# Performance work log

Hardware: AMD Instinct MI355X
Metric: run time of the kernel (lower is better)

The kernel has to match this reference:

```python
import jax, jax.numpy as jnp
import numpy as np

B, H, W = 8, 64, 64
DIM, NH, WS = 384, 6, 14
HD = DIM // NH
MLP = int(DIM * 4.0)
EPS = 1e-5
SCALE = HD ** -0.5


def setup_inputs() -> dict:
    key = jax.random.key(0)
    ks = jax.random.split(key, 8)
    init = lambda k, shape: (jax.random.normal(k, shape, dtype=jnp.float32) * 0.02)
    return {
        "x": jax.random.normal(ks[0], (B, H, W, DIM), dtype=jnp.float32),
        "ln1_w": jnp.ones((DIM,), jnp.float32),
        "ln1_b": jnp.zeros((DIM,), jnp.float32),
        "qkv_w": init(ks[1], (DIM, 3 * DIM)),
        "qkv_b": jnp.zeros((3 * DIM,), jnp.float32),
        "proj_w": init(ks[2], (DIM, DIM)),
        "proj_b": jnp.zeros((DIM,), jnp.float32),
        "rel_pos_h": init(ks[3], (2 * WS - 1, HD)),
        "rel_pos_w": init(ks[4], (2 * WS - 1, HD)),
        "ln2_w": jnp.ones((DIM,), jnp.float32),
        "ln2_b": jnp.zeros((DIM,), jnp.float32),
        "fc1_w": init(ks[5], (DIM, MLP)),
        "fc1_b": jnp.zeros((MLP,), jnp.float32),
        "fc2_w": init(ks[6], (MLP, DIM)),
        "fc2_b": jnp.zeros((DIM,), jnp.float32),
    }


def _layernorm(x, w, b):
    m = x.mean(-1, keepdims=True)
    v = ((x - m) ** 2).mean(-1, keepdims=True)
    return (x - m) * jax.lax.rsqrt(v + EPS) * w + b


def _get_rel_pos(rel_pos, ws):
    # q_size == k_size == ws and rel_pos has 2*ws-1 rows, so torch's
    # F.interpolate to max_rel_dist=2*ws-1 is an identity; direct indexing.
    coords = jnp.arange(ws)[:, None] - jnp.arange(ws)[None, :] + (ws - 1)
    return rel_pos[coords]  # (ws, ws, head_dim)


def _attention(xw, qkv_w, qkv_b, proj_w, proj_b, rel_pos_h, rel_pos_w):
    Bw = xw.shape[0]
    N = WS * WS
    qkv = xw.reshape(Bw, N, DIM) @ qkv_w + qkv_b  # (Bw, N, 3*DIM)
    qkv = qkv.reshape(Bw, N, 3, NH, HD).transpose(2, 0, 3, 1, 4).reshape(3, Bw * NH, N, HD)
    q, k, v = qkv[0], qkv[1], qkv[2]
    attn = jnp.einsum("bqd,bkd->bqk", q * SCALE, k)  # (Bw*NH, N, N)
    Rh = _get_rel_pos(rel_pos_h, WS)
    Rw = _get_rel_pos(rel_pos_w, WS)
    rq = q.reshape(Bw * NH, WS, WS, HD)
    rel_h = jnp.einsum("bhwc,hkc->bhwk", rq, Rh)
    rel_w = jnp.einsum("bhwc,wkc->bhwk", rq, Rw)
    attn = (attn.reshape(Bw * NH, WS, WS, WS, WS)
            + rel_h[:, :, :, :, None]
            + rel_w[:, :, :, None, :]).reshape(Bw * NH, N, N)
    attn = jax.nn.softmax(attn, axis=-1)
    out = jnp.einsum("bqk,bkd->bqd", attn, v)
    out = out.reshape(Bw, NH, WS, WS, HD).transpose(0, 2, 3, 1, 4).reshape(Bw, WS, WS, DIM)
    return out @ proj_w + proj_b


def reference(x, ln1_w, ln1_b, qkv_w, qkv_b, proj_w, proj_b, rel_pos_h, rel_pos_w,
              ln2_w, ln2_b, fc1_w, fc1_b, fc2_w, fc2_b):
    shortcut = x
    h = _layernorm(x, ln1_w, ln1_b)
    pad_h = (WS - H % WS) % WS
    pad_w = (WS - W % WS) % WS
    Hp, Wp = H + pad_h, W + pad_w
    hp = jnp.pad(h, ((0, 0), (0, pad_h), (0, pad_w), (0, 0)))
    # window partition: (B, Hp, Wp, C) -> (B*nWin, WS, WS, C)
    wins = hp.reshape(B, Hp // WS, WS, Wp // WS, WS, DIM)
    wins = wins.transpose(0, 1, 3, 2, 4, 5).reshape(-1, WS, WS, DIM)
    wins = _attention(wins, qkv_w, qkv_b, proj_w, proj_b, rel_pos_h, rel_pos_w)
    # window unpartition
    y = wins.reshape(B, Hp // WS, Wp // WS, WS, WS, DIM)
    y = y.transpose(0, 1, 3, 2, 4, 5).reshape(B, Hp, Wp, DIM)[:, :H, :W, :]
    x = shortcut + y
    h2 = _layernorm(x, ln2_w, ln2_b)
    mlp = jax.nn.gelu(h2 @ fc1_w + fc1_b, approximate=False) @ fc2_w + fc2_b
    return x + mlp
```

## Files before the change

kernel.cpp:

```cpp
#include <hip/hip_runtime.h>
#include <math.h>

#define DIMC 384
#define NHD  6
#define HD   64
#define WSZ  14
#define NTOK 196
#define NWIN 200
#define NWH  1200
#define MWIN 39200
#define MX   32768
#define MLPD 1536

typedef short short8 __attribute__((ext_vector_type(8)));
typedef float f32x4 __attribute__((ext_vector_type(4)));
typedef float f32x16 __attribute__((ext_vector_type(16)));

__device__ __forceinline__ unsigned short f2bf(float f) {
  unsigned int u = __float_as_uint(f);
  u = (u + 0x7fffu + ((u >> 16) & 1u)) >> 16;
  return (unsigned short)u;
}
__device__ __forceinline__ unsigned int pkbf(float a, float b) {
  unsigned int r; asm("v_cvt_pk_bf16_f32 %0, %1, %2" : "=v"(r) : "v"(a), "v"(b)); return r;
}
__device__ __forceinline__ float gelu_t(float x) {
  float z = 1.5957691216057308f * (x + 0.044715f * x * x * x);
  float e = __expf(z);
  float th = 1.f - 2.f * __builtin_amdgcn_rcpf(e + 1.f);
  return 0.5f * x * (1.f + th);
}

typedef const __attribute__((address_space(1))) unsigned int* gptr_t;
typedef __attribute__((address_space(3))) unsigned int* lptr_t;
__device__ __forceinline__ void gload16(const unsigned short* g, unsigned short* l) {
  __builtin_amdgcn_global_load_lds((gptr_t)(const void*)g, (lptr_t)(void*)l, 16, 0, 0);
}

__global__ void wtrans_kernel(const float* __restrict__ in, unsigned short* __restrict__ out,
                              int K, int N) {
  int id = blockIdx.x * 256 + threadIdx.x;
  if (id >= K * N) return;
  int n = id / K, k = id - n * K;
  out[id] = f2bf(in[(size_t)k * N + n]);
}

__global__ void relprep_kernel(const float* __restrict__ relh, const float* __restrict__ relw,
                               unsigned short* __restrict__ relcat) {
  int id = blockIdx.x * 256 + threadIdx.x;
  if (id >= 64 * 64) return;
  int rc = id >> 6, d = id & 63;
  float v = 0.f;
  if (rc < 27) v = relh[rc * 64 + d] * 8.f;
  else if (rc < 54) v = relw[(rc - 27) * 64 + d] * 8.f;
  relcat[id] = f2bf(v);
}

__global__ void vpad_kernel(unsigned short* __restrict__ vT) {
  int id = blockIdx.x * 256 + threadIdx.x;
  if (id >= 76800 * 3) return;
  int row = id / 3, part = id - row * 3;
  *(int2*)(vT + (size_t)row * 208 + 196 + part * 4) = make_int2(0, 0);
}

__global__ __launch_bounds__(64) void ln1win_kernel(const float* __restrict__ x,
    const float* __restrict__ w, const float* __restrict__ b, unsigned short* __restrict__ xw) {
  int t = blockIdx.x;
  int lane = threadIdx.x;
  int win = t / NTOK, p = t - win * NTOK;
  int bb = win / 25, rem = win - bb * 25;
  int wi = rem / 5, wj = rem - wi * 5;
  int i = p / WSZ, j = p - i * WSZ;
  int r = wi * WSZ + i, c = wj * WSZ + j;
  unsigned short* o = xw + (size_t)t * DIMC;
  if (r >= 64 || c >= 64) {
    #pragma unroll
    for (int q = 0; q < 6; q++) o[lane + q * 64] = 0;
    return;
  }
  const float* xr = x + (((size_t)bb * 64 + r) * 64 + c) * DIMC;
  float v[6]; float s = 0.f, s2 = 0.f;
  #pragma unroll
  for (int q = 0; q < 6; q++) { float f = xr[lane + q * 64]; v[q] = f; s += f; s2 += f * f; }
  #pragma unroll
  for (int off = 32; off; off >>= 1) { s += __shfl_xor(s, off); s2 += __shfl_xor(s2, off); }
  float mean = s * (1.f / DIMC);
  float var  = s2 * (1.f / DIMC) - mean * mean;
  float rstd = rsqrtf(var + 1e-5f);
  #pragma unroll
  for (int q = 0; q < 6; q++) {
    int d = lane + q * 64;
    o[d] = f2bf((v[q] - mean) * rstd * w[d] + b[d]);
  }
}

__global__ __launch_bounds__(64) void ln2_kernel(const float* __restrict__ x2,
    const float* __restrict__ w, const float* __restrict__ b, unsigned short* __restrict__ h2) {
  int t = blockIdx.x; int lane = threadIdx.x;
  const float* xr = x2 + (size_t)t * DIMC;
  unsigned short* o = h2 + (size_t)t * DIMC;
  float v[6]; float s = 0.f, s2 = 0.f;
  #pragma unroll
  for (int q = 0; q < 6; q++) { float f = xr[lane + q * 64]; v[q] = f; s += f; s2 += f * f; }
  #pragma unroll
  for (int off = 32; off; off >>= 1) { s += __shfl_xor(s, off); s2 += __shfl_xor(s2, off); }
  float mean = s * (1.f / DIMC);
  float var  = s2 * (1.f / DIMC) - mean * mean;
  float rstd = rsqrtf(var + 1e-5f);
  #pragma unroll
  for (int q = 0; q < 6; q++) {
    int d = lane + q * 64;
    o[d] = f2bf((v[q] - mean) * rstd * w[d] + b[d]);
  }
}

template <int EPI>
__global__ __launch_bounds__(256) void gemm_kernel(
    const unsigned short* __restrict__ A, const unsigned short* __restrict__ WT,
    int Mrows, int Kd,
    const float* __restrict__ bias, const float* __restrict__ addin,
    float* __restrict__ outf, unsigned short* __restrict__ outb,
    unsigned short* __restrict__ outb2) {
  __shared__ unsigned short As[3][128 * 32];
  __shared__ unsigned short Bs[3][128 * 32];
  const int nwg = gridDim.x * gridDim.y;
  const int flat = blockIdx.y * gridDim.x + blockIdx.x;
  const int xcd = flat & 7, q_ = nwg >> 3, r_ = nwg & 7;
  const int wg = (xcd < r_ ? xcd * (q_ + 1) : r_ * (q_ + 1) + (xcd - r_) * q_) + (flat >> 3);
  const int bx = wg / gridDim.y, by = wg - bx * gridDim.y;
  const int row0 = bx * 128, col0 = by * 128;
  const int tid = threadIdx.x;
  const int l = tid & 63, wid = tid >> 6;
  const int fr = l & 15, fk = (l >> 4) * 8;
  const int wr = (wid >> 1) * 64, wc = (wid & 1) * 64;
  const int sr = l >> 2, sc = (l & 3) * 8;
  const int scs = sc ^ (((sr >> 1) & 3) << 3);
  const int rsw = ((fr >> 1) & 3) << 3;
  f32x4 acc[4][4] = {};
  const unsigned short* ap = A + (size_t)row0 * Kd;
  const unsigned short* bp = WT + (size_t)col0 * Kd;
  const int nt = Kd >> 5;

  auto stage = [&](int t, int b) {
    const int k0 = t * 32;
    #pragma unroll
    for (int j = 0; j < 2; j++) {
      int chunk = j * 4 + wid;
      gload16(ap + (size_t)(chunk * 16 + sr) * Kd + k0 + scs, &As[b][chunk * 512]);
      gload16(bp + (size_t)(chunk * 16 + sr) * Kd + k0 + scs, &Bs[b][chunk * 512]);
    }
  };
  stage(0, 0);
  stage(1, 1);
  int c = 0;
  for (int t = 0; t < nt; ++t) {
    if (t < nt - 1) asm volatile("s_waitcnt vmcnt(4)" ::: "memory");
    else            asm volatile("s_waitcnt vmcnt(0)" ::: "memory");
    __builtin_amdgcn_s_barrier();
    __builtin_amdgcn_sched_barrier(0);
    if (t + 2 < nt) stage(t + 2, (c + 2 >= 3) ? c - 1 : c + 2);
    short8 a[4], b[4];
    #pragma unroll
    for (int fi = 0; fi < 4; fi++) {
      a[fi] = *(const short8*)&As[c][(wr + fi * 16 + fr) * 32 + (fk ^ rsw)];
      b[fi] = *(const short8*)&Bs[c][(wc + fi * 16 + fr) * 32 + (fk ^ rsw)];
    }
    __builtin_amdgcn_s_setprio(1);
    #pragma unroll
    for (int fi = 0; fi < 4; fi++)
      #pragma unroll
      for (int fj = 0; fj < 4; fj++)
        acc[fi][fj] = __builtin_amdgcn_mfma_f32_16x16x32_bf16(b[fj], a[fi], acc[fi][fj], 0, 0, 0);
    __builtin_amdgcn_s_setprio(0);
    c = (c + 1 >= 3) ? 0 : c + 1;
  }
  #pragma unroll
  for (int fi = 0; fi < 4; fi++) {
    const int gr = row0 + wr + fi * 16 + fr;
    if (gr >= Mrows) continue;
    int wv_ = 0, p = 0, valid = 1; size_t pixbase = 0;
    if (EPI == 0 || EPI == 1) { wv_ = gr / NTOK; p = gr - wv_ * NTOK; }
    if (EPI == 1) {
      int bb = wv_ / 25, rem2 = wv_ - bb * 25;
      int wi = rem2 / 5, wj = rem2 - wi * 5;
      int i = p / WSZ, j = p - i * WSZ;
      int rr = wi * WSZ + i, cc = wj * WSZ + j;
      valid = (rr < 64) && (cc < 64);
      pixbase = (((size_t)bb * 64 + rr) * 64 + cc) * DIMC;
    }
    #pragma unroll
    for (int fj = 0; fj < 4; fj++) {
      const int gcb = col0 + wc + fj * 16 + (l >> 4) * 4;
      f32x4 v = acc[fi][fj];
      float4 bv = *(const float4*)&bias[gcb];
      float t0 = v[0] + bv.x, t1 = v[1] + bv.y, t2 = v[2] + bv.z, t3 = v[3] + bv.w;
      if (EPI == 0) {
        int s = gcb / 384, rem = gcb - s * 384;
        int hh = rem >> 6, d0 = gcb & 63;
        int whh = wv_ * NHD + hh;
        if (s == 0) { t0 *= 0.125f; t1 *= 0.125f; t2 *= 0.125f; t3 *= 0.125f; }
        if (s < 2) {
          *(int2*)&outb[((size_t)s * NWH + whh) * (NTOK * 64) + p * 64 + d0] =
              make_int2((int)pkbf(t0, t1), (int)pkbf(t2, t3));
        } else {
          unsigned short* vb = outb2 + ((size_t)whh * 64 + d0) * 208 + p;
          vb[0] = f2bf(t0); vb[208] = f2bf(t1); vb[416] = f2bf(t2); vb[624] = f2bf(t3);
        }
      } else if (EPI == 1) {
        if (valid) {
          size_t idx = pixbase + gcb;
          float4 ad = *(const float4*)&addin[idx];
          *(float4*)&outf[idx] = make_float4(t0 + ad.x, t1 + ad.y, t2 + ad.z, t3 + ad.w);
        }
      } else if (EPI == 2) {
        *(int2*)&outb[(size_t)gr * MLPD + gcb] =
            make_int2((int)pkbf(gelu_t(t0), gelu_t(t1)), (int)pkbf(gelu_t(t2), gelu_t(t3)));
      } else {
        size_t idx = (size_t)gr * DIMC + gcb;
        float4 ad = *(const float4*)&addin[idx];
        *(float4*)&outf[idx] = make_float4(t0 + ad.x, t1 + ad.y, t2 + ad.z, t3 + ad.w);
      }
    }
  }
}

template <bool TAIL>
__device__ __forceinline__ void attn_chunk(
    int kk, int l31, int hi,
    const unsigned short* __restrict__ kg,
    const unsigned short* __restrict__ VT,
    const short8* qf, const short8* qrel,
    f32x16& olo, f32x16& ohi_, float& m_reg, float& s_run) {
  int key = kk * 32 + l31;
  int keyc = (TAIL && key > 195) ? 195 : key;
  f32x16 S = {};
  __builtin_amdgcn_s_setprio(1);
  #pragma unroll
  for (int m = 0; m < 4; m++) {
    short8 kf = *(const short8*)(kg + (size_t)keyc * 64 + m * 16 + hi * 8);
    S = __builtin_amdgcn_mfma_f32_32x32x16_bf16(kf, qf[m], S, 0, 0, 0);
  }
  {
    int ki = keyc / 14, kj = keyc - ki * 14;
    #pragma unroll
    for (int m2 = 0; m2 < 2; m2++) {
      short8 kh;
      #pragma unroll
      for (int j = 0; j < 8; j++) {
        int cc = m2 * 16 + hi * 8 + j;
        kh[j] = (short)((cc == ki || cc == 14 + kj) ? 0x3F80 : 0);
      }
      S = __builtin_amdgcn_mfma_f32_32x32x16_bf16(kh, qrel[m2], S, 0, 0, 0);
    }
  }
  __builtin_amdgcn_s_setprio(0);
  float pmax = -3e38f;
  #pragma unroll
  for (int r = 0; r < 16; r++) {
    if (TAIL) {
      int krow = kk * 32 + (r & 3) + 8 * (r >> 2) + 4 * hi;
      if (krow >= 196) S[r] = -3e38f;
    }
    pmax = fmaxf(pmax, S[r]);
  }
  pmax = fmaxf(pmax, __shfl_xor(pmax, 32));
  if (__any(pmax > m_reg + 8.f)) {
    float m_new = fmaxf(m_reg, pmax);
    float fac = __expf(m_reg - m_new);
    m_reg = m_new;
    s_run *= fac;
    #pragma unroll
    for (int r = 0; r < 16; r++) {
      int qr = (r & 3) + 8 * (r >> 2) + 4 * hi;
      float fr_ = __shfl(fac, qr);
      olo[r] *= fr_; ohi_[r] *= fr_;
    }
  }
  float psum = 0.f;
  #pragma unroll
  for (int r = 0; r < 16; r++) { S[r] = __expf(S[r] - m_reg); psum += S[r]; }
  s_run += psum;
  unsigned int pk[8];
  #pragma unroll
  for (int t = 0; t < 8; t++) pk[t] = pkbf(S[2 * t], S[2 * t + 1]);
  #pragma unroll
  for (int m2 = 0; m2 < 2; m2++) {
    int b_ = m2 * 4;
    unsigned int x0 = (unsigned int)__shfl_xor((int)pk[b_ + 0], 32);
    unsigned int x1 = (unsigned int)__shfl_xor((int)pk[b_ + 1], 32);
    unsigned int x2 = (unsigned int)__shfl_xor((int)pk[b_ + 2], 32);
    unsigned int x3 = (unsigned int)__shfl_xor((int)pk[b_ + 3], 32);
    unsigned int au[4];
    au[0] = hi ? x2 : pk[b_ + 0];
    au[1] = hi ? x3 : pk[b_ + 1];
    au[2] = hi ? pk[b_ + 2] : x0;
    au[3] = hi ? pk[b_ + 3] : x1;
    short8 pa; __builtin_memcpy(&pa, au, 16);
    int kb = kk * 32 + m2 * 16 + hi * 8;
    if (TAIL && kb > 208) kb = 208;
    short8 vblo = *(const short8*)&VT[l31 * 216 + kb];
    short8 vbhi = *(const short8*)&VT[(32 + l31) * 216 + kb];
    __builtin_amdgcn_s_setprio(1);
    olo  = __builtin_amdgcn_mfma_f32_32x32x16_bf16(pa, vblo, olo, 0, 0, 0);
    ohi_ = __builtin_amdgcn_mfma_f32_32x32x16_bf16(pa, vbhi, ohi_, 0, 0, 0);
    __builtin_amdgcn_s_setprio(0);
  }
}

__global__ __launch_bounds__(256) void attn32_kernel(
    const unsigned short* __restrict__ qk_g,
    const unsigned short* __restrict__ vT_g,
    const unsigned short* __restrict__ relcat,
    unsigned short* __restrict__ attnout) {
  __shared__ __align__(16) unsigned short VT[64 * 216];
  __shared__ __align__(16) unsigned short RELB[4][2048];
  const int wh = blockIdx.x;
  const int w = wh / NHD, h = wh - w * NHD;
  const int tid = threadIdx.x;
  const unsigned short* vrow = vT_g + (size_t)wh * 64 * 208;
  for (int e = tid; e < 64 * 27; e += 256) {
    int d = e / 27, c = e - d * 27;
    int4 val = {0, 0, 0, 0};
    if (c < 26) val = *(const int4*)(vrow + d * 208 + c * 8);
    *(int4*)&VT[d * 216 + c * 8] = val;
  }
  __syncthreads();
  const int l = tid & 63, wv = tid >> 6;
  const int l31 = l & 31, hi = l >> 5;
  unsigned short* RB = &RELB[wv][0];
  const unsigned short* qg = qk_g + (size_t)wh * (NTOK * 64);
  const unsigned short* kg = qk_g + (size_t)(NWH + wh) * (NTOK * 64);

  for (int tile = wv; tile < 7; tile += 4) {
    const int q0 = tile * 32;
    int qrow = q0 + l31; if (qrow > 195) qrow = 195;
    short8 qf[4];
    #pragma unroll
    for (int m = 0; m < 4; m++)
      qf[m] = *(const short8*)(qg + (size_t)qrow * 64 + m * 16 + hi * 8);
    #pragma unroll
    for (int rt = 0; rt < 2; rt++) {
      f32x16 cr = {};
      __builtin_amdgcn_s_setprio(1);
      #pragma unroll
      for (int m = 0; m < 4; m++) {
        short8 af = *(const short8*)(relcat + (rt * 32 + l31) * 64 + m * 16 + hi * 8);
        cr = __builtin_amdgcn_mfma_f32_32x32x16_bf16(af, qf[m], cr, 0, 0, 0);
      }
      __builtin_amdgcn_s_setprio(0);
      #pragma unroll
      for (int t = 0; t < 8; t++) {
        int rr = rt * 32 + ((2 * t) & 3) + 8 * (t >> 1) + 4 * hi;
        *(unsigned int*)&RB[l31 * 64 + rr] = pkbf(cr[2 * t], cr[2 * t + 1]);
      }
    }
    __builtin_amdgcn_wave_barrier();
    int qi = qrow / 14, qj = qrow - qi * 14;
    short8 qrel[2];
    #pragma unroll
    for (int m2 = 0; m2 < 2; m2++)
      #pragma unroll
      for (int j = 0; j < 8; j++) {
        int cc = m2 * 16 + hi * 8 + j;
        unsigned short vv = 0;
        if (cc < 14) vv = RB[l31 * 64 + (qi - cc + 13)];
        else if (cc < 28) vv = RB[l31 * 64 + 27 + (qj - (cc - 14) + 13)];
        qrel[m2][j] = (short)vv;
      }
    __builtin_amdgcn_wave_barrier();
    f32x16 olo = {}, ohi_ = {};
    float m_reg = -3e38f, s_run = 0.f;
    for (int kk = 0; kk < 6; kk++)
      attn_chunk<false>(kk, l31, hi, kg, VT, qf, qrel, olo, ohi_, m_reg, s_run);
    attn_chunk<true>(6, l31, hi, kg, VT, qf, qrel, olo, ohi_, m_reg, s_run);
    s_run += __shfl_xor(s_run, 32);
    float inv = 1.f / s_run;
    #pragma unroll
    for (int r = 0; r < 16; r++) {
      int qr = (r & 3) + 8 * (r >> 2) + 4 * hi;
      float ir = __shfl(inv, qr);
      int tok = q0 + qr;
      if (tok < 196) {
        size_t base = ((size_t)w * NTOK + tok) * DIMC + h * 64;
        attnout[base + l31] = f2bf(olo[r] * ir);
        attnout[base + 32 + l31] = f2bf(ohi_[r] * ir);
      }
    }
  }
}

extern "C" void kernel_launch(void* const* d_in, const int* in_sizes, int n_in,
                              void* d_out, int out_size, void* d_ws, size_t ws_size,
                              hipStream_t stream) {
  const float* x     = (const float*)d_in[0];
  const float* ln1w  = (const float*)d_in[1];
  const float* ln1b  = (const float*)d_in[2];
  const float* qkvw  = (const float*)d_in[3];
  const float* qkvb  = (const float*)d_in[4];
  const float* projw = (const float*)d_in[5];
  const float* projb = (const float*)d_in[6];
  const float* relh  = (const float*)d_in[7];
  const float* relw  = (const float*)d_in[8];
  const float* ln2w  = (const float*)d_in[9];
  const float* ln2b  = (const float*)d_in[10];
  const float* fc1w  = (const float*)d_in[11];
  const float* fc1b  = (const float*)d_in[12];
  const float* fc2w  = (const float*)d_in[13];
  const float* fc2b  = (const float*)d_in[14];

  const size_t R0 = 0;
  const size_t R1 = R0 + 50331648;
  const size_t R2 = R1 + 100663296;
  const size_t R3 = R2 + 30408704;
  const size_t NEED = R3 + 3547136;
  if (ws_size < NEED) return;
  char* ws = (char*)d_ws;
  unsigned short* xw     = (unsigned short*)(ws + R0);
  float*          x2     = (float*)(ws + R0);
  unsigned short* qk_g   = (unsigned short*)(ws + R1);
  unsigned short* vT_g   = qk_g + (size_t)2 * NWH * NTOK * 64;
  unsigned short* hidden = (unsigned short*)(ws + R1);
  unsigned short* attno  = (unsigned short*)(ws + R2);
  unsigned short* h2     = (unsigned short*)(ws + R2);
  unsigned short* qkvwT  = (unsigned short*)(ws + R3);
  unsigned short* projwT = qkvwT + 442368;
  unsigned short* fc1wT  = projwT + 147456;
  unsigned short* fc2wT  = fc1wT + 589824;
  unsigned short* relcat = fc2wT + 589824;

  wtrans_kernel<<<1728, 256, 0, stream>>>(qkvw, qkvwT, 384, 1152);
  wtrans_kernel<<<576, 256, 0, stream>>>(projw, projwT, 384, 384);
  wtrans_kernel<<<2304, 256, 0, stream>>>(fc1w, fc1wT, 384, 1536);
  wtrans_kernel<<<2304, 256, 0, stream>>>(fc2w, fc2wT, 1536, 384);
  relprep_kernel<<<16, 256, 0, stream>>>(relh, relw, relcat);
  vpad_kernel<<<900, 256, 0, stream>>>(vT_g);
  ln1win_kernel<<<MWIN, 64, 0, stream>>>(x, ln1w, ln1b, xw);
  gemm_kernel<0><<<dim3(307, 9), 256, 0, stream>>>(xw, qkvwT, MWIN, 384, qkvb, nullptr, nullptr, qk_g, vT_g);
  attn32_kernel<<<NWH, 256, 0, stream>>>(qk_g, vT_g, relcat, attno);
  gemm_kernel<1><<<dim3(307, 3), 256, 0, stream>>>(attno, projwT, MWIN, 384, projb, x, x2, nullptr, nullptr);
  ln2_kernel<<<MX, 64, 0, stream>>>(x2, ln2w, ln2b, h2);
  gemm_kernel<2><<<dim3(256, 12), 256, 0, stream>>>(h2, fc1wT, MX, 384, fc1b, nullptr, nullptr, hidden, nullptr);
  gemm_kernel<3><<<dim3(256, 3), 256, 0, stream>>>(hidden, fc2wT, MX, 1536, fc2b, x2, (float*)d_out, nullptr, nullptr);
}
```

Measured before the change: 359.5 us.

## Switch GEMMs to 256x256 tiles with 8 waves and ping-pong interleaved pipeline

Rewrites the shared GEMM kernel to use 256x256 output tiles with 512 threads (8 waves), K-step 64, and a double-buffered LDS scheme. Within each K step, A and B fragment loads are interleaved with four MFMA phases separated by barriers, and global prefetches are spread across those phases. The goal is more arithmetic per byte loaded and better overlap of loads with MFMA work. In exchange it uses more registers and LDS per block, launches fewer blocks, and needs column bounds checks plus enlarged weight buffers so N can be padded to a multiple of 256.

```diff
diff --git a/kernel.cpp b/kernel.cpp
--- a/kernel.cpp
+++ b/kernel.cpp
@@ -115,68 +115,119 @@
 }
 
 template <int EPI>
-__global__ __launch_bounds__(256) void gemm_kernel(
+__global__ __launch_bounds__(512) void gemm_kernel(
     const unsigned short* __restrict__ A, const unsigned short* __restrict__ WT,
-    int Mrows, int Kd,
+    int Mrows, int Ncols, int Kd,
     const float* __restrict__ bias, const float* __restrict__ addin,
     float* __restrict__ outf, unsigned short* __restrict__ outb,
     unsigned short* __restrict__ outb2) {
-  __shared__ unsigned short As[3][128 * 32];
-  __shared__ unsigned short Bs[3][128 * 32];
+  __shared__ __align__(16) unsigned short As[2][2][8192];
+  __shared__ __align__(16) unsigned short Bs[2][2][8192];
   const int nwg = gridDim.x * gridDim.y;
   const int flat = blockIdx.y * gridDim.x + blockIdx.x;
   const int xcd = flat & 7, q_ = nwg >> 3, r_ = nwg & 7;
   const int wg = (xcd < r_ ? xcd * (q_ + 1) : r_ * (q_ + 1) + (xcd - r_) * q_) + (flat >> 3);
   const int bx = wg / gridDim.y, by = wg - bx * gridDim.y;
-  const int row0 = bx * 128, col0 = by * 128;
+  const int row0 = bx * 256, col0 = by * 256;
   const int tid = threadIdx.x;
   const int l = tid & 63, wid = tid >> 6;
-  const int fr = l & 15, fk = (l >> 4) * 8;
-  const int wr = (wid >> 1) * 64, wc = (wid & 1) * 64;
-  const int sr = l >> 2, sc = (l & 3) * 8;
-  const int scs = sc ^ (((sr >> 1) & 3) << 3);
-  const int rsw = ((fr >> 1) & 3) << 3;
-  f32x4 acc[4][4] = {};
+  const int wid_m = wid >> 2, wid_n = wid & 3;
+  const int fr = l & 15, fq = l >> 4;
+  const int rsw = (fr & 7) * 8;
+  const int ch = wid * 2;
+  const int scol = ((l & 7) * 8) ^ (l & 56);
   const unsigned short* ap = A + (size_t)row0 * Kd;
   const unsigned short* bp = WT + (size_t)col0 * Kd;
-  const int nt = Kd >> 5;
-
-  auto stage = [&](int t, int b) {
-    const int k0 = t * 32;
+  const int nt = Kd >> 6;
+
+  auto stageA = [&](int kt, int half) {
     #pragma unroll
     for (int j = 0; j < 2; j++) {
-      int chunk = j * 4 + wid;
-      gload16(ap + (size_t)(chunk * 16 + sr) * Kd + k0 + scs, &As[b][chunk * 512]);
-      gload16(bp + (size_t)(chunk * 16 + sr) * Kd + k0 + scs, &Bs[b][chunk * 512]);
+      int c = ch + j;
+      gload16(ap + (size_t)(half * 128 + c * 8 + (l >> 3)) * Kd + kt * 64 + scol,
+              &As[kt & 1][half][c * 512]);
     }
   };
-  stage(0, 0);
-  stage(1, 1);
-  int c = 0;
+  auto stageB = [&](int kt, int half) {
+    #pragma unroll
+    for (int j = 0; j < 2; j++) {
+      int c = ch + j;
+      gload16(bp + (size_t)(half * 128 + c * 8 + (l >> 3)) * Kd + kt * 64 + scol,
+              &Bs[kt & 1][half][c * 512]);
+    }
+  };
+
+  f32x4 acc[8][4] = {};
+  short8 a[8], b01[4], b23[4];
+
+  auto lda = [&](int buf, int rbase) {
+    #pragma unroll
+    for (int f = 0; f < 4; f++)
+      #pragma unroll
+      for (int kk = 0; kk < 2; kk++)
+        a[f * 2 + kk] = *(const short8*)
+            &As[buf][wid_m][((rbase + f) * 16 + fr) * 64 + ((kk * 32 + fq * 8) ^ rsw)];
+  };
+  auto ldb = [&](short8* bf, int buf, int cbase) {
+    const int halfb = wid_n >> 1, rb = (wid_n & 1) * 64;
+    #pragma unroll
+    for (int f = 0; f < 2; f++)
+      #pragma unroll
+      for (int kk = 0; kk < 2; kk++)
+        bf[f * 2 + kk] = *(const short8*)
+            &Bs[buf][halfb][(rb + (cbase + f) * 16 + fr) * 64 + ((kk * 32 + fq * 8) ^ rsw)];
+  };
+
+#define MMA(bf, aset, bset)                                                               \
+  __builtin_amdgcn_s_setprio(1);                                                          \
+  _Pragma("unroll")                                                                       \
+  for (int f = 0; f < 4; f++)                                                             \
+    _Pragma("unroll")                                                                     \
+    for (int g = 0; g < 2; g++)                                                           \
+      _Pragma("unroll")                                                                   \
+      for (int kk = 0; kk < 2; kk++)                                                      \
+        acc[(aset) * 4 + f][(bset) * 2 + g] = __builtin_amdgcn_mfma_f32_16x16x32_bf16(    \
+            bf[g * 2 + kk], a[f * 2 + kk], acc[(aset) * 4 + f][(bset) * 2 + g], 0, 0, 0); \
+  __builtin_amdgcn_s_setprio(0);
+
+#define FENCE asm volatile("" ::: "memory")
+#define BAR   __builtin_amdgcn_s_barrier()
+
+  stageA(0, 0); stageA(0, 1); stageB(0, 0); stageB(0, 1);
+  stageB(1, 0); stageB(1, 1);
+  asm volatile("s_waitcnt vmcnt(4)" ::: "memory");
+  BAR;
   for (int t = 0; t < nt; ++t) {
-    if (t < nt - 1) asm volatile("s_waitcnt vmcnt(4)" ::: "memory");
+    const int buf = t & 1;
+    lda(buf, 0); ldb(b01, buf, 0);
+    if (t + 1 < nt) stageA(t + 1, 0);
+    FENCE; BAR;
+    MMA(b01, 0, 0);
+    FENCE; BAR;
+    ldb(b23, buf, 2);
+    if (t + 1 < nt) stageA(t + 1, 1);
+    FENCE; BAR;
+    MMA(b23, 0, 1);
+    FENCE; BAR;
+    lda(buf, 4);
+    if (t + 2 < nt) stageB(t + 2, 0);
+    FENCE; BAR;
+    MMA(b23, 1, 1);
+    FENCE; BAR;
+    if (t + 2 < nt) stageB(t + 2, 1);
+    FENCE; BAR;
+    MMA(b01, 1, 0);
+    if (t < nt - 2) asm volatile("s_waitcnt vmcnt(4)" ::: "memory");
     else            asm volatile("s_waitcnt vmcnt(0)" ::: "memory");
-    __builtin_amdgcn_s_barrier();
-    __builtin_amdgcn_sched_barrier(0);
-    if (t + 2 < nt) stage(t + 2, (c + 2 >= 3) ? c - 1 : c + 2);
-    short8 a[4], b[4];
-    #pragma unroll
-    for (int fi = 0; fi < 4; fi++) {
-      a[fi] = *(const short8*)&As[c][(wr + fi * 16 + fr) * 32 + (fk ^ rsw)];
-      b[fi] = *(const short8*)&Bs[c][(wc + fi * 16 + fr) * 32 + (fk ^ rsw)];
-    }
-    __builtin_amdgcn_s_setprio(1);
-    #pragma unroll
-    for (int fi = 0; fi < 4; fi++)
-      #pragma unroll
-      for (int fj = 0; fj < 4; fj++)
-        acc[fi][fj] = __builtin_amdgcn_mfma_f32_16x16x32_bf16(b[fj], a[fi], acc[fi][fj], 0, 0, 0);
-    __builtin_amdgcn_s_setprio(0);
-    c = (c + 1 >= 3) ? 0 : c + 1;
-  }
-  #pragma unroll
-  for (int fi = 0; fi < 4; fi++) {
-    const int gr = row0 + wr + fi * 16 + fr;
+    BAR;
+  }
+#undef MMA
+#undef FENCE
+#undef BAR
+
+  #pragma unroll
+  for (int fi = 0; fi < 8; fi++) {
+    const int gr = row0 + wid_m * 128 + fi * 16 + fr;
     if (gr >= Mrows) continue;
     int wv_ = 0, p = 0, valid = 1; size_t pixbase = 0;
     if (EPI == 0 || EPI == 1) { wv_ = gr / NTOK; p = gr - wv_ * NTOK; }
@@ -190,7 +241,8 @@
     }
     #pragma unroll
     for (int fj = 0; fj < 4; fj++) {
-      const int gcb = col0 + wc + fj * 16 + (l >> 4) * 4;
+      const int gcb = col0 + wid_n * 64 + fj * 16 + fq * 4;
+      if (gcb >= Ncols) continue;
       f32x4 v = acc[fi][fj];
       float4 bv = *(const float4*)&bias[gcb];
       float t0 = v[0] + bv.x, t1 = v[1] + bv.y, t2 = v[2] + bv.z, t3 = v[3] + bv.w;
@@ -412,7 +464,7 @@
   const size_t R1 = R0 + 50331648;
   const size_t R2 = R1 + 100663296;
   const size_t R3 = R2 + 30408704;
-  const size_t NEED = R3 + 3547136;
+  const size_t NEED = R3 + 4136960;
   if (ws_size < NEED) return;
   char* ws = (char*)d_ws;
   unsigned short* xw     = (unsigned short*)(ws + R0);
@@ -423,10 +475,10 @@
   unsigned short* attno  = (unsigned short*)(ws + R2);
   unsigned short* h2     = (unsigned short*)(ws + R2);
   unsigned short* qkvwT  = (unsigned short*)(ws + R3);
-  unsigned short* projwT = qkvwT + 442368;
-  unsigned short* fc1wT  = projwT + 147456;
+  unsigned short* projwT = qkvwT + 491520;
+  unsigned short* fc1wT  = projwT + 196608;
   unsigned short* fc2wT  = fc1wT + 589824;
-  unsigned short* relcat = fc2wT + 589824;
+  unsigned short* relcat = fc2wT + 786432;
 
   wtrans_kernel<<<1728, 256, 0, stream>>>(qkvw, qkvwT, 384, 1152);
   wtrans_kernel<<<576, 256, 0, stream>>>(projw, projwT, 384, 384);
@@ -435,10 +487,10 @@
   relprep_kernel<<<16, 256, 0, stream>>>(relh, relw, relcat);
   vpad_kernel<<<900, 256, 0, stream>>>(vT_g);
   ln1win_kernel<<<MWIN, 64, 0, stream>>>(x, ln1w, ln1b, xw);
-  gemm_kernel<0><<<dim3(307, 9), 256, 0, stream>>>(xw, qkvwT, MWIN, 384, qkvb, nullptr, nullptr, qk_g, vT_g);
+  gemm_kernel<0><<<dim3(154, 5), 512, 0, stream>>>(xw, qkvwT, MWIN, 1152, 384, qkvb, nullptr, nullptr, qk_g, vT_g);
   attn32_kernel<<<NWH, 256, 0, stream>>>(qk_g, vT_g, relcat, attno);
-  gemm_kernel<1><<<dim3(307, 3), 256, 0, stream>>>(attno, projwT, MWIN, 384, projb, x, x2, nullptr, nullptr);
+  gemm_kernel<1><<<dim3(154, 2), 512, 0, stream>>>(attno, projwT, MWIN, 384, 384, projb, x, x2, nullptr, nullptr);
   ln2_kernel<<<MX, 64, 0, stream>>>(x2, ln2w, ln2b, h2);
-  gemm_kernel<2><<<dim3(256, 12), 256, 0, stream>>>(h2, fc1wT, MX, 384, fc1b, nullptr, nullptr, hidden, nullptr);
-  gemm_kernel<3><<<dim3(256, 3), 256, 0, stream>>>(hidden, fc2wT, MX, 1536, fc2b, x2, (float*)d_out, nullptr, nullptr);
-}
+  gemm_kernel<2><<<dim3(128, 6), 512, 0, stream>>>(h2, fc1wT, MX, 1536, 384, fc1b, nullptr, nullptr, hidden, nullptr);
+  gemm_kernel<3><<<dim3(128, 2), 512, 0, stream>>>(hidden, fc2wT, MX, 384, 1536, fc2b, x2, (float*)d_out, nullptr, nullptr);
+}
```

Result: slower. 403.3 us (+12.2%).
